# Kernel tuning notes

Measured on AMD Instinct MI355X. Metric: run time of the kernel, lower is better.

The kernel has to match this reference:

```python
import jax, jax.numpy as jnp
import numpy as np

N = 1_000_000          # number of RoIs
C = 4                  # num_class (foreground classes)
IMG_H, IMG_W = 1080.0, 1920.0
BBOX_MEAN = jnp.array([0.0, 0.0, 0.0, 0.0], jnp.float32)
BBOX_STD = jnp.array([0.1, 0.1, 0.2, 0.2], jnp.float32)
THR_OBJ = 0.2          # threshold_objectness
THR_CLS = 0.1          # thresholds[0]
MIN_W, MIN_H = 6.0, 6.0
MAX_CAND = 300         # nms max_candidate_n
OVERLAP = 0.5          # nms overlap_ratio
TOP_N = 100            # nms top_n


def setup_inputs() -> dict:
    key = jax.random.key(0)
    k1, k2, k3, k4, k5 = jax.random.split(key, 5)
    logits = jax.random.normal(k1, (N, C + 1), jnp.float32) * 2.0
    cls_score_softmax = jax.nn.softmax(logits, axis=-1)          # rows sum to 1, like softmax output
    bbox_pred = jax.random.normal(k2, (N, 4 * (C + 1)), jnp.float32) * 0.5
    x1 = jax.random.uniform(k3, (N,), jnp.float32, 0.0, IMG_W * 0.8)
    y1 = jax.random.uniform(k4, (N,), jnp.float32, 0.0, IMG_H * 0.8)
    wh = jax.random.uniform(k5, (N, 2), jnp.float32, 8.0, 200.0)
    rois = jnp.stack([jnp.zeros((N,), jnp.float32), x1, y1, x1 + wh[:, 0], y1 + wh[:, 1]], axis=1)
    im_info = jnp.array([IMG_H, IMG_W], jnp.float32)
    return {"cls_score_softmax": cls_score_softmax, "bbox_pred": bbox_pred, "rois": rois, "im_info": im_info}


def _pairwise_iou(b):
    # torchvision box_iou convention: area = (x2-x1)*(y2-y1), no +1
    lt = jnp.maximum(b[:, None, :2], b[None, :, :2])
    rb = jnp.minimum(b[:, None, 2:], b[None, :, 2:])
    wh = jnp.clip(rb - lt, 0.0)
    inter = wh[..., 0] * wh[..., 1]
    area = (b[:, 2] - b[:, 0]) * (b[:, 3] - b[:, 1])
    return inter / (area[:, None] + area[None, :] - inter)


def _forward(cls_score_softmax, bbox_pred, rois, im_info):
    h_img, w_img = im_info[0], im_info[1]
    # denormalize deltas and decode against rois (bbox_transform_inv_rcnn)
    deltas = (bbox_pred.reshape(-1, 4) * BBOX_STD + BBOX_MEAN).reshape(-1, C + 1, 4)
    bx = rois[:, 1:]
    w = bx[:, 2] - bx[:, 0] + 1.0
    h = bx[:, 3] - bx[:, 1] + 1.0
    cx = bx[:, 0] + 0.5 * (w - 1.0)
    cy = bx[:, 1] + 0.5 * (h - 1.0)
    pcx = deltas[:, :, 0] * w[:, None] + cx[:, None]
    pcy = deltas[:, :, 1] * h[:, None] + cy[:, None]
    pw = jnp.exp(deltas[:, :, 2]) * w[:, None]
    ph = jnp.exp(deltas[:, :, 3]) * h[:, None]
    pred = jnp.stack([pcx - 0.5 * (pw - 1.0), pcy - 0.5 * (ph - 1.0),
                      pcx + 0.5 * (pw - 1.0), pcy + 0.5 * (ph - 1.0)], axis=-1)  # [N, C+1, 4]
    # refine_out_of_map_bbox: clip to image
    pred = jnp.stack([jnp.clip(pred[..., 0], 0.0, w_img - 1.0),
                      jnp.clip(pred[..., 1], 0.0, h_img - 1.0),
                      jnp.clip(pred[..., 2], 0.0, w_img - 1.0),
                      jnp.clip(pred[..., 3], 0.0, h_img - 1.0)], axis=-1)
    # objectness + class-score filters (masked instead of compacted: jit-friendly)
    mask_obj = (1.0 - cls_score_softmax[:, 0]) >= THR_OBJ
    maxes = jnp.max(cls_score_softmax[:, 1:], axis=1)
    argmaxes = jnp.argmax(cls_score_softmax[:, 1:], axis=1) + 1
    mask_cls = maxes > THR_CLS
    # select the box of the argmax class per row
    box = jnp.take_along_axis(pred, argmaxes[:, None, None], axis=1)[:, 0, :]  # [N, 4]
    bw = box[:, 2] - box[:, 0] + 1.0
    bh = box[:, 3] - box[:, 1] + 1.0
    mask_size = (bw >= MIN_W) | (bh >= MIN_H)  # HEIGHT_OR_WIDTH
    valid = mask_obj & mask_cls & mask_size
    # top-k candidates by max class prob (invalid rows pushed below any real score)
    cand_scores = jnp.where(valid, maxes, -1.0)
    top_vals, top_idx = jax.lax.top_k(cand_scores, MAX_CAND)   # sorted descending
    cand_boxes = box[top_idx]                                   # [M, 4]
    cand_probs = cls_score_softmax[top_idx]                     # [M, C+1]
    cand_valid = top_vals > -0.5
    # greedy NMS over the (score-sorted) candidates
    iou = _pairwise_iou(cand_boxes)
    idx = jnp.arange(MAX_CAND)

    def body(i, keep):
        sup = keep[i] & (iou[i] > OVERLAP) & (idx > i)
        return keep & ~sup

    keep = jax.lax.fori_loop(0, MAX_CAND, body, cand_valid)
    # compact kept rows into the first TOP_N slots (drop-row scatter trick)
    order = jnp.cumsum(keep.astype(jnp.int32)) - 1
    slot = jnp.where(keep & (order < TOP_N), order, TOP_N)
    rows = jnp.concatenate([jnp.zeros((MAX_CAND, 1), cand_boxes.dtype), cand_boxes, cand_probs], axis=1)
    out = jnp.zeros((TOP_N + 1, rows.shape[1]), rows.dtype).at[slot].set(rows)[:TOP_N]
    return out  # [TOP_N, 1 + 4 + (C+1)] = [100, 10], zero-padded past the kept count


def reference(cls_score_softmax, bbox_pred, rois, im_info):
    return _forward(cls_score_softmax, bbox_pred, rois, im_info)
```

## Files before the change

### kernel.cpp

```cpp
#include <hip/hip_runtime.h>
#include <math.h>

#define NBINS 4096
#define CAP   4096
#define MAXC  300
#define MAXCP 320
#define NTASK (MAXC*5)
#define TOPN  100

__device__ __forceinline__ void decode4(float x1, float y1, float x2, float y2,
                                        float4 d4, float Wimg, float Himg,
                                        float& bx1, float& by1, float& bx2, float& by2)
{
    float w  = x2 - x1 + 1.0f;
    float h  = y2 - y1 + 1.0f;
    float cx = x1 + 0.5f*(w - 1.0f);
    float cy = y1 + 0.5f*(h - 1.0f);
    float d0 = d4.x*0.1f, d1 = d4.y*0.1f, d2 = d4.z*0.2f, d3 = d4.w*0.2f;
    float pcx = d0*w + cx;
    float pcy = d1*h + cy;
    float pw  = expf(d2)*w;
    float ph  = expf(d3)*h;
    bx1 = fminf(fmaxf(pcx - 0.5f*(pw-1.0f), 0.0f), Wimg-1.0f);
    by1 = fminf(fmaxf(pcy - 0.5f*(ph-1.0f), 0.0f), Himg-1.0f);
    bx2 = fminf(fmaxf(pcx + 0.5f*(pw-1.0f), 0.0f), Wimg-1.0f);
    by2 = fminf(fmaxf(pcy + 0.5f*(ph-1.0f), 0.0f), Himg-1.0f);
}

__global__ __launch_bounds__(256)
void rcnn_pass1(const float4* __restrict__ cls4, const float4* __restrict__ bbox4,
                const float4* __restrict__ rois4, const float* __restrict__ iminfo,
                float4* __restrict__ scores4,
                unsigned int* __restrict__ hist, unsigned int* __restrict__ counter, int Ng)
{
    if (blockIdx.x == 0) {
        for (int k = threadIdx.x; k < NBINS; k += 256) hist[k] = 0u;
        if (threadIdx.x == 0) *counter = 0u;
    }

    int g = blockIdx.x * blockDim.x + threadIdx.x;
    if (g >= Ng) return;

    float c[20], q[20];
    #pragma unroll
    for (int v = 0; v < 5; v++) {
        float4 cv = cls4[5*g + v];
        c[4*v] = cv.x; c[4*v+1] = cv.y; c[4*v+2] = cv.z; c[4*v+3] = cv.w;
        float4 rv = rois4[5*g + v];
        q[4*v] = rv.x; q[4*v+1] = rv.y; q[4*v+2] = rv.z; q[4*v+3] = rv.w;
    }
    float Himg = iminfo[0], Wimg = iminfo[1];

    float s[4];
    #pragma unroll
    for (int j = 0; j < 4; j++) {
        float p0 = c[5*j], p1 = c[5*j+1], p2 = c[5*j+2], p3 = c[5*j+3], p4 = c[5*j+4];
        float m = p1; int a = 1;
        if (p2 > m) { m = p2; a = 2; }
        if (p3 > m) { m = p3; a = 3; }
        if (p4 > m) { m = p4; a = 4; }
        float sc = -1.0f;
        if (((1.0f - p0) >= 0.2f) && (m > 0.1f)) {
            float4 d4 = bbox4[20*g + 5*j + a];
            float bx1, by1, bx2, by2;
            decode4(q[5*j+1], q[5*j+2], q[5*j+3], q[5*j+4], d4, Wimg, Himg, bx1, by1, bx2, by2);
            float bw = bx2 - bx1 + 1.0f;
            float bh = by2 - by1 + 1.0f;
            if ((bw >= 6.0f) || (bh >= 6.0f)) sc = m;
        }
        s[j] = sc;
    }
    scores4[g] = make_float4(s[0], s[1], s[2], s[3]);
}

__global__ __launch_bounds__(1024)
void rcnn_hist(const float4* __restrict__ scores4, unsigned int* __restrict__ hist, int Ng)
{
    __shared__ unsigned int lh[NBINS];
    const int t = threadIdx.x;
    for (int k = t; k < NBINS; k += 1024) lh[k] = 0u;
    __syncthreads();

    int stride = gridDim.x * 1024;
    for (int g = blockIdx.x * 1024 + t; g < Ng; g += stride) {
        float4 s4 = scores4[g];
        float ss[4] = { s4.x, s4.y, s4.z, s4.w };
        #pragma unroll
        for (int j = 0; j < 4; j++) {
            float s = ss[j];
            if (s > -0.5f) {
                int bin = (int)(s * (float)NBINS);
                bin = bin > NBINS-1 ? NBINS-1 : bin;
                atomicAdd(&lh[bin], 1u);
            }
        }
    }
    __syncthreads();
    for (int k = t; k < NBINS; k += 1024) {
        unsigned int v = lh[k];
        if (v) atomicAdd(&hist[k], v);
    }
}

__global__ __launch_bounds__(64)
void rcnn_pass2(const unsigned int* __restrict__ hist, int* __restrict__ taubin)
{
    const int t = threadIdx.x;
    const uint4* h4 = (const uint4*)hist;
    uint4 v[16];
    #pragma unroll
    for (int j = 0; j < 16; j++) v[j] = h4[t*16 + j];
    unsigned int chunk = 0;
    #pragma unroll
    for (int j = 0; j < 16; j++) chunk += v[j].x + v[j].y + v[j].z + v[j].w;

    unsigned int sfx = chunk;
    #pragma unroll
    for (int d = 1; d < 64; d <<= 1) {
        unsigned int o = __shfl_down(sfx, d, 64);
        if (t + d < 64) sfx += o;
    }
    unsigned int nxt = sfx - chunk;
    bool found = (sfx >= MAXC) && (nxt < MAXC);
    unsigned long long bal = __ballot(found);
    if (found) {
        unsigned int cum = nxt;
        int tau = 64*t;
        #pragma unroll
        for (int k = 15; k >= 0; k--) {
            cum += v[k].w; if (cum >= MAXC) { tau = 64*t + 4*k + 3; goto done; }
            cum += v[k].z; if (cum >= MAXC) { tau = 64*t + 4*k + 2; goto done; }
            cum += v[k].y; if (cum >= MAXC) { tau = 64*t + 4*k + 1; goto done; }
            cum += v[k].x; if (cum >= MAXC) { tau = 64*t + 4*k + 0; goto done; }
        }
        done:
        *taubin = tau;
    }
    if (bal == 0ull && t == 0) *taubin = 0;
}

__global__ __launch_bounds__(256)
void rcnn_pass3(const float4* __restrict__ scores4, const int* __restrict__ taubin,
                float* __restrict__ cscore, int* __restrict__ cidx,
                unsigned int* __restrict__ counter, int Ng)
{
    int g = blockIdx.x * blockDim.x + threadIdx.x;
    if (g >= Ng) return;
    float4 s4 = scores4[g];
    int tau = *taubin;
    float ss[4] = { s4.x, s4.y, s4.z, s4.w };
    #pragma unroll
    for (int j = 0; j < 4; j++) {
        float s = ss[j];
        if (s > -0.5f) {
            int bin = (int)(s * (float)NBINS);
            bin = bin > NBINS-1 ? NBINS-1 : bin;
            if (bin >= tau) {
                unsigned int pos = atomicAdd(counter, 1u);
                if (pos < CAP) { cscore[pos] = s; cidx[pos] = 4*g + j; }
            }
        }
    }
}

__global__ __launch_bounds__(1024)
void rcnn_rank(const float* __restrict__ cls, const float* __restrict__ bbox,
               const float* __restrict__ rois, const float* __restrict__ iminfo,
               const float* __restrict__ cscore, const int* __restrict__ cidx,
               const unsigned int* __restrict__ counter,
               float4* __restrict__ bxg, float* __restrict__ areag,
               float* __restrict__ prg, unsigned long long* __restrict__ maskg)
{
    __shared__ __align__(16) float s_s[CAP];
    __shared__ __align__(16) int   s_id[CAP];
    __shared__ int tid_[MAXC];
    __shared__ unsigned long long maskw[5];
    const int t  = threadIdx.x;
    const int NT = 1024;
    int M = (int)*counter; if (M > CAP) M = CAP;

    for (int i = t; i < M; i += NT)  { s_s[i] = cscore[i]; s_id[i] = cidx[i]; }
    for (int r = t; r < MAXC; r += NT) tid_[r] = -1;
    if (t < 5) maskw[t] = 0ull;
    __syncthreads();

    {
        const float4* sv = (const float4*)s_s;
        const int4*   dv = (const int4*)s_id;
        int M4 = M >> 2;
        for (int i = t; i < M; i += NT) {
            float si = s_s[i]; int di = s_id[i];
            int r = 0;
            for (int jj = 0; jj < M4; jj++) {
                float4 sj = sv[jj]; int4 dj = dv[jj];
                r += (sj.x > si) || (sj.x == si && dj.x < di);
                r += (sj.y > si) || (sj.y == si && dj.y < di);
                r += (sj.z > si) || (sj.z == si && dj.z < di);
                r += (sj.w > si) || (sj.w == si && dj.w < di);
            }
            for (int j = M4 << 2; j < M; j++) {
                float sj = s_s[j]; int dj = s_id[j];
                r += (sj > si) || (sj == si && dj < di);
            }
            if (r < MAXC) tid_[r] = di;
        }
    }
    __syncthreads();

    float Himg = iminfo[0], Wimg = iminfo[1];
    for (int r = t; r < MAXCP; r += NT) {
        int i = (r < MAXC) ? tid_[r] : -1;
        float4 bx = make_float4(0.0f, 0.0f, 0.0f, 0.0f);
        float ar = 0.0f;
        if (i >= 0) {
            float p0 = cls[5*i], p1 = cls[5*i+1], p2 = cls[5*i+2], p3 = cls[5*i+3], p4 = cls[5*i+4];
            prg[5*r+0]=p0; prg[5*r+1]=p1; prg[5*r+2]=p2; prg[5*r+3]=p3; prg[5*r+4]=p4;
            float m = p1; int a = 1;
            if (p2 > m) { m = p2; a = 2; }
            if (p3 > m) { m = p3; a = 3; }
            if (p4 > m) { m = p4; a = 4; }
            float4 d4 = ((const float4*)bbox)[5*i + a];
            float bx1, by1, bx2, by2;
            decode4(rois[5*i+1], rois[5*i+2], rois[5*i+3], rois[5*i+4], d4, Wimg, Himg, bx1, by1, bx2, by2);
            bx = make_float4(bx1, by1, bx2, by2);
            ar = (bx2-bx1)*(by2-by1);
            atomicOr(&maskw[r>>6], 1ull << (r & 63));
        }
        bxg[r] = bx; areag[r] = ar;
    }
    __syncthreads();
    if (t < 5) maskg[t] = maskw[t];
}

__global__ __launch_bounds__(64)
void rcnn_sup(const float4* __restrict__ bxg, const float* __restrict__ areag,
              const unsigned long long* __restrict__ maskg,
              unsigned long long* __restrict__ supg)
{
    __shared__ float4 bxs[MAXCP];
    __shared__ float  ars[MAXCP];
    const int t = threadIdx.x;
    for (int r = t; r < MAXCP; r += 64) { bxs[r] = bxg[r]; ars[r] = areag[r]; }
    __syncthreads();

    int task = blockIdx.x * 64 + t;
    if (task >= NTASK) return;
    int w = task / MAXC;
    int i = task - w * MAXC;
    unsigned long long bits = 0ull;
    int j0 = w << 6;
    if (j0 + 63 > i) {
        float4 bi = bxs[i];
        float areaA = ars[i];
        for (int b = 0; b < 64; b++) {
            int j = j0 + b;
            float4 bj = bxs[j];
            float lx = fmaxf(bi.x, bj.x), ly = fmaxf(bi.y, bj.y);
            float rx = fminf(bi.z, bj.z), ry = fminf(bi.w, bj.w);
            float iw = fmaxf(rx - lx, 0.0f), ih = fmaxf(ry - ly, 0.0f);
            float inter = iw * ih;
            float iou = inter / (areaA + ars[j] - inter);
            bits |= (iou > 0.5f) ? (1ull << b) : 0ull;
        }
        unsigned long long jgt = (i < j0) ? ~0ull
                              : ((i - j0) >= 63 ? 0ull : ~((1ull << (i - j0 + 1)) - 1ull));
        bits &= jgt & maskg[w];
    }
    supg[i*6 + w] = bits;
}

__global__ __launch_bounds__(1024)
void rcnn_scan(const float4* __restrict__ bxg, const float* __restrict__ prg,
               const unsigned long long* __restrict__ maskg,
               const unsigned long long* __restrict__ supg, float* __restrict__ out)
{
    __shared__ __align__(16) unsigned long long sup[MAXC*6];
    __shared__ unsigned long long maskw[5];
    __shared__ float orows[TOPN*10];
    __shared__ int   kept_list[TOPN];
    __shared__ int   s_kept;
    const int t  = threadIdx.x;
    const int NT = 1024;

    {
        const ulonglong2* sg2 = (const ulonglong2*)supg;
        ulonglong2* sl2 = (ulonglong2*)sup;
        for (int k = t; k < (MAXC*6)/2; k += NT) sl2[k] = sg2[k];
    }
    if (t < 5) maskw[t] = maskg[t];
    for (int k = t; k < TOPN*10; k += NT) orows[k] = 0.0f;
    __syncthreads();

    if (t == 0) {
        unsigned long long k0=maskw[0], k1=maskw[1], k2=maskw[2], k3=maskw[3], k4=maskw[4];
        int kept = 0;
        #define SCAN_WORD(W, KW)                                                   \
        if (kept < TOPN) {                                                         \
            unsigned long long donem = 0ull;                                       \
            for (;;) {                                                             \
                unsigned long long rem = (KW) & ~donem;                            \
                if (!rem) break;                                                   \
                int b = __builtin_ctzll(rem);                                      \
                int i = (W << 6) + b;                                              \
                kept_list[kept++] = i;                                             \
                if (kept >= TOPN) break;                                           \
                unsigned long long s0 = sup[i*6+0], s1 = sup[i*6+1],               \
                                   s2 = sup[i*6+2], s3 = sup[i*6+3],               \
                                   s4 = sup[i*6+4];                                \
                k0 &= ~s0; k1 &= ~s1; k2 &= ~s2; k3 &= ~s3; k4 &= ~s4;             \
                donem = (b == 63) ? ~0ull : ((2ull << b) - 1ull);                  \
            }                                                                      \
        }
        SCAN_WORD(0, k0)
        SCAN_WORD(1, k1)
        SCAN_WORD(2, k2)
        SCAN_WORD(3, k3)
        SCAN_WORD(4, k4)
        #undef SCAN_WORD
        s_kept = kept;
    }
    __syncthreads();

    int kept = s_kept;
    if (t < kept) {
        int r = kept_list[t];
        float4 bx = bxg[r];
        float* row = &orows[t*10];
        row[0] = 0.0f;
        row[1] = bx.x; row[2] = bx.y; row[3] = bx.z; row[4] = bx.w;
        row[5] = prg[5*r+0]; row[6] = prg[5*r+1]; row[7] = prg[5*r+2];
        row[8] = prg[5*r+3]; row[9] = prg[5*r+4];
    }
    __syncthreads();
    for (int k = t; k < TOPN*10; k += NT) out[k] = orows[k];
}

extern "C" void kernel_launch(void* const* d_in, const int* in_sizes, int n_in,
                              void* d_out, int out_size, void* d_ws, size_t ws_size,
                              hipStream_t stream)
{
    const float* cls    = (const float*)d_in[0];
    const float* bbox   = (const float*)d_in[1];
    const float* rois   = (const float*)d_in[2];
    const float* iminfo = (const float*)d_in[3];
    int N  = in_sizes[0] / 5;
    int Ng = N / 4;

    char* ws = (char*)d_ws;
    float* scores = (float*)ws;
    size_t off = ((size_t)N * 4 + 255) & ~(size_t)255;
    unsigned int* hist    = (unsigned int*)(ws + off); off += NBINS * 4;
    int*          taubin  = (int*)(ws + off);          off += 256;
    unsigned int* counter = (unsigned int*)(ws + off); off += 256;
    float*        cscore  = (float*)(ws + off);        off += CAP * 4;
    int*          cidx    = (int*)(ws + off);          off += CAP * 4;
    float4*       bxg     = (float4*)(ws + off);       off += MAXCP * 16;
    float*        areag   = (float*)(ws + off);        off += ((MAXCP * 4 + 255) & ~(size_t)255);
    float*        prg     = (float*)(ws + off);        off += ((MAXC * 5 * 4 + 255) & ~(size_t)255);
    unsigned long long* maskg = (unsigned long long*)(ws + off); off += 256;
    unsigned long long* supg  = (unsigned long long*)(ws + off); off += MAXC * 6 * 8;

    int blocksG = (Ng + 255) / 256;
    rcnn_pass1<<<blocksG, 256, 0, stream>>>((const float4*)cls, (const float4*)bbox,
                                            (const float4*)rois, iminfo,
                                            (float4*)scores, hist, counter, Ng);
    rcnn_hist<<<64, 1024, 0, stream>>>((const float4*)scores, hist, Ng);
    rcnn_pass2<<<1, 64, 0, stream>>>(hist, taubin);
    rcnn_pass3<<<blocksG, 256, 0, stream>>>((const float4*)scores, taubin,
                                            cscore, cidx, counter, Ng);
    rcnn_rank<<<1, 1024, 0, stream>>>(cls, bbox, rois, iminfo,
                                      cscore, cidx, counter,
                                      bxg, areag, prg, maskg);
    rcnn_sup<<<(NTASK + 63) / 64, 64, 0, stream>>>(bxg, areag, maskg, supg);
    rcnn_scan<<<1, 1024, 0, stream>>>(bxg, prg, maskg, supg, (float*)d_out);
}
```

Before: 206.5 us.

## Fuse seven launches into three using grid-wide atomic tickets and spin barriers

```diff
diff --git a/kernel.cpp b/kernel.cpp
--- a/kernel.cpp
+++ b/kernel.cpp
@@ -7,6 +7,8 @@
 #define MAXCP 320
 #define NTASK (MAXC*5)
 #define TOPN  100
+#define HBLK  64
+#define RBLK  25
 
 __device__ __forceinline__ void decode4(float x1, float y1, float x2, float y2,
                                         float4 d4, float Wimg, float Himg,
@@ -30,17 +32,24 @@
 __global__ __launch_bounds__(256)
 void rcnn_pass1(const float4* __restrict__ cls4, const float4* __restrict__ bbox4,
                 const float4* __restrict__ rois4, const float* __restrict__ iminfo,
-                float4* __restrict__ scores4,
-                unsigned int* __restrict__ hist, unsigned int* __restrict__ counter, int Ng)
+                float4* __restrict__ scores4, unsigned int* __restrict__ hist,
+                int* __restrict__ taubin, unsigned int* __restrict__ hticket,
+                unsigned int* __restrict__ counter, unsigned int* __restrict__ rtick,
+                unsigned int* __restrict__ stick,
+                float4* __restrict__ bxg, float* __restrict__ areag,
+                unsigned long long* __restrict__ maskg, int Ng)
 {
     if (blockIdx.x == 0) {
         for (int k = threadIdx.x; k < NBINS; k += 256) hist[k] = 0u;
-        if (threadIdx.x == 0) *counter = 0u;
-    }
-
+        if (threadIdx.x == 0) { *counter = 0u; *hticket = 0u; *rtick = 0u; *stick = 0u; *taubin = -1; }
+        if (threadIdx.x < 5) maskg[threadIdx.x] = 0ull;
+        for (int r = threadIdx.x; r < MAXCP; r += 256) {
+            bxg[r] = make_float4(0.0f, 0.0f, 0.0f, 0.0f);
+            areag[r] = 0.0f;
+        }
+    }
     int g = blockIdx.x * blockDim.x + threadIdx.x;
     if (g >= Ng) return;
-
     float c[20], q[20];
     #pragma unroll
     for (int v = 0; v < 5; v++) {
@@ -50,7 +59,6 @@
         q[4*v] = rv.x; q[4*v+1] = rv.y; q[4*v+2] = rv.z; q[4*v+3] = rv.w;
     }
     float Himg = iminfo[0], Wimg = iminfo[1];
-
     float s[4];
     #pragma unroll
     for (int j = 0; j < 4; j++) {
@@ -74,13 +82,17 @@
 }
 
 __global__ __launch_bounds__(1024)
-void rcnn_hist(const float4* __restrict__ scores4, unsigned int* __restrict__ hist, int Ng)
+void rcnn_histc(const float4* __restrict__ scores4, unsigned int* __restrict__ hist,
+                unsigned int* __restrict__ hticket, int* __restrict__ taubin,
+                float* __restrict__ cscore, int* __restrict__ cidx,
+                unsigned int* __restrict__ counter, int Ng)
 {
     __shared__ unsigned int lh[NBINS];
+    __shared__ unsigned int s_tick;
+    __shared__ int s_tau;
     const int t = threadIdx.x;
     for (int k = t; k < NBINS; k += 1024) lh[k] = 0u;
     __syncthreads();
-
     int stride = gridDim.x * 1024;
     for (int g = blockIdx.x * 1024 + t; g < Ng; g += stride) {
         float4 s4 = scores4[g];
@@ -100,239 +112,243 @@
         unsigned int v = lh[k];
         if (v) atomicAdd(&hist[k], v);
     }
-}
-
-__global__ __launch_bounds__(64)
-void rcnn_pass2(const unsigned int* __restrict__ hist, int* __restrict__ taubin)
-{
-    const int t = threadIdx.x;
-    const uint4* h4 = (const uint4*)hist;
-    uint4 v[16];
-    #pragma unroll
-    for (int j = 0; j < 16; j++) v[j] = h4[t*16 + j];
-    unsigned int chunk = 0;
-    #pragma unroll
-    for (int j = 0; j < 16; j++) chunk += v[j].x + v[j].y + v[j].z + v[j].w;
-
-    unsigned int sfx = chunk;
-    #pragma unroll
-    for (int d = 1; d < 64; d <<= 1) {
-        unsigned int o = __shfl_down(sfx, d, 64);
-        if (t + d < 64) sfx += o;
-    }
-    unsigned int nxt = sfx - chunk;
-    bool found = (sfx >= MAXC) && (nxt < MAXC);
-    unsigned long long bal = __ballot(found);
-    if (found) {
-        unsigned int cum = nxt;
-        int tau = 64*t;
+
+    __threadfence();
+    __syncthreads();
+    if (t == 0) s_tick = atomicAdd(hticket, 1u);
+    __syncthreads();
+
+    if (s_tick == gridDim.x - 1) {
+        __threadfence();
+        if (t < 64) {
+            const uint4* h4 = (const uint4*)hist;
+            uint4 v[16];
+            #pragma unroll
+            for (int j = 0; j < 16; j++) v[j] = h4[t*16 + j];
+            unsigned int chunk = 0;
+            #pragma unroll
+            for (int j = 0; j < 16; j++) chunk += v[j].x + v[j].y + v[j].z + v[j].w;
+            unsigned int sfx = chunk;
+            #pragma unroll
+            for (int d = 1; d < 64; d <<= 1) {
+                unsigned int o = __shfl_down(sfx, d, 64);
+                if (t + d < 64) sfx += o;
+            }
+            unsigned int nxt = sfx - chunk;
+            bool found = (sfx >= MAXC) && (nxt < MAXC);
+            unsigned long long bal = __ballot(found);
+            if (found) {
+                unsigned int cum = nxt;
+                int tauv = 64*t;
+                #pragma unroll
+                for (int k = 15; k >= 0; k--) {
+                    cum += v[k].w; if (cum >= MAXC) { tauv = 64*t + 4*k + 3; goto dtau; }
+                    cum += v[k].z; if (cum >= MAXC) { tauv = 64*t + 4*k + 2; goto dtau; }
+                    cum += v[k].y; if (cum >= MAXC) { tauv = 64*t + 4*k + 1; goto dtau; }
+                    cum += v[k].x; if (cum >= MAXC) { tauv = 64*t + 4*k + 0; goto dtau; }
+                }
+                dtau:
+                atomicExch(taubin, tauv);
+            }
+            if (bal == 0ull && t == 0) atomicExch(taubin, 0);
+        }
+    }
+
+    if (t == 0) {
+        int tv = atomicAdd(taubin, 0);
+        while (tv < 0) { __builtin_amdgcn_s_sleep(2); tv = atomicAdd(taubin, 0); }
+        s_tau = tv;
+    }
+    __syncthreads();
+    int tau = s_tau;
+
+    for (int g = blockIdx.x * 1024 + t; g < Ng; g += stride) {
+        float4 s4 = scores4[g];
+        float ss[4] = { s4.x, s4.y, s4.z, s4.w };
         #pragma unroll
-        for (int k = 15; k >= 0; k--) {
-            cum += v[k].w; if (cum >= MAXC) { tau = 64*t + 4*k + 3; goto done; }
-            cum += v[k].z; if (cum >= MAXC) { tau = 64*t + 4*k + 2; goto done; }
-            cum += v[k].y; if (cum >= MAXC) { tau = 64*t + 4*k + 1; goto done; }
-            cum += v[k].x; if (cum >= MAXC) { tau = 64*t + 4*k + 0; goto done; }
-        }
-        done:
-        *taubin = tau;
-    }
-    if (bal == 0ull && t == 0) *taubin = 0;
-}
-
-__global__ __launch_bounds__(256)
-void rcnn_pass3(const float4* __restrict__ scores4, const int* __restrict__ taubin,
-                float* __restrict__ cscore, int* __restrict__ cidx,
-                unsigned int* __restrict__ counter, int Ng)
-{
-    int g = blockIdx.x * blockDim.x + threadIdx.x;
-    if (g >= Ng) return;
-    float4 s4 = scores4[g];
-    int tau = *taubin;
-    float ss[4] = { s4.x, s4.y, s4.z, s4.w };
-    #pragma unroll
-    for (int j = 0; j < 4; j++) {
-        float s = ss[j];
-        if (s > -0.5f) {
-            int bin = (int)(s * (float)NBINS);
-            bin = bin > NBINS-1 ? NBINS-1 : bin;
-            if (bin >= tau) {
-                unsigned int pos = atomicAdd(counter, 1u);
-                if (pos < CAP) { cscore[pos] = s; cidx[pos] = 4*g + j; }
+        for (int j = 0; j < 4; j++) {
+            float s = ss[j];
+            if (s > -0.5f) {
+                int bin = (int)(s * (float)NBINS);
+                bin = bin > NBINS-1 ? NBINS-1 : bin;
+                if (bin >= tau) {
+                    unsigned int pos = atomicAdd(counter, 1u);
+                    if (pos < CAP) { cscore[pos] = s; cidx[pos] = 4*g + j; }
+                }
             }
         }
     }
 }
 
 __global__ __launch_bounds__(1024)
-void rcnn_rank(const float* __restrict__ cls, const float* __restrict__ bbox,
-               const float* __restrict__ rois, const float* __restrict__ iminfo,
-               const float* __restrict__ cscore, const int* __restrict__ cidx,
-               const unsigned int* __restrict__ counter,
-               float4* __restrict__ bxg, float* __restrict__ areag,
-               float* __restrict__ prg, unsigned long long* __restrict__ maskg)
-{
-    __shared__ __align__(16) float s_s[CAP];
-    __shared__ __align__(16) int   s_id[CAP];
-    __shared__ int tid_[MAXC];
-    __shared__ unsigned long long maskw[5];
-    const int t  = threadIdx.x;
-    const int NT = 1024;
-    int M = (int)*counter; if (M > CAP) M = CAP;
-
-    for (int i = t; i < M; i += NT)  { s_s[i] = cscore[i]; s_id[i] = cidx[i]; }
-    for (int r = t; r < MAXC; r += NT) tid_[r] = -1;
-    if (t < 5) maskw[t] = 0ull;
-    __syncthreads();
+void rcnn_mega2(const float* __restrict__ cls, const float* __restrict__ bbox,
+                const float* __restrict__ rois, const float* __restrict__ iminfo,
+                const float* __restrict__ cscore, const int* __restrict__ cidx,
+                const unsigned int* __restrict__ counter,
+                unsigned int* __restrict__ rtick, unsigned int* __restrict__ stick,
+                float4* __restrict__ bxg, float* __restrict__ areag,
+                float* __restrict__ prg, unsigned long long* __restrict__ maskg,
+                unsigned long long* __restrict__ supg, float* __restrict__ out)
+{
+    __shared__ __align__(16) unsigned char u[32768];
+    __shared__ float orows[TOPN*10];
+    __shared__ int   kept_list[TOPN];
+    __shared__ int   s_kept;
+    const int t   = threadIdx.x;
+    const int bid = blockIdx.x;
 
     {
+        float* s_s  = (float*)u;
+        int*   s_id = (int*)(u + CAP*4);
+        int M = (int)*counter; if (M > CAP) M = CAP;
+        for (int i = t; i < M; i += 1024) { s_s[i] = cscore[i]; s_id[i] = cidx[i]; }
+        __syncthreads();
+        int C = (M + RBLK - 1) / RBLK;
+        float Himg = iminfo[0], Wimg = iminfo[1];
         const float4* sv = (const float4*)s_s;
         const int4*   dv = (const int4*)s_id;
         int M4 = M >> 2;
-        for (int i = t; i < M; i += NT) {
-            float si = s_s[i]; int di = s_id[i];
-            int r = 0;
-            for (int jj = 0; jj < M4; jj++) {
-                float4 sj = sv[jj]; int4 dj = dv[jj];
-                r += (sj.x > si) || (sj.x == si && dj.x < di);
-                r += (sj.y > si) || (sj.y == si && dj.y < di);
-                r += (sj.z > si) || (sj.z == si && dj.z < di);
-                r += (sj.w > si) || (sj.w == si && dj.w < di);
-            }
-            for (int j = M4 << 2; j < M; j++) {
-                float sj = s_s[j]; int dj = s_id[j];
-                r += (sj > si) || (sj == si && dj < di);
-            }
-            if (r < MAXC) tid_[r] = di;
-        }
-    }
-    __syncthreads();
-
-    float Himg = iminfo[0], Wimg = iminfo[1];
-    for (int r = t; r < MAXCP; r += NT) {
-        int i = (r < MAXC) ? tid_[r] : -1;
-        float4 bx = make_float4(0.0f, 0.0f, 0.0f, 0.0f);
-        float ar = 0.0f;
-        if (i >= 0) {
-            float p0 = cls[5*i], p1 = cls[5*i+1], p2 = cls[5*i+2], p3 = cls[5*i+3], p4 = cls[5*i+4];
-            prg[5*r+0]=p0; prg[5*r+1]=p1; prg[5*r+2]=p2; prg[5*r+3]=p3; prg[5*r+4]=p4;
-            float m = p1; int a = 1;
-            if (p2 > m) { m = p2; a = 2; }
-            if (p3 > m) { m = p3; a = 3; }
-            if (p4 > m) { m = p4; a = 4; }
-            float4 d4 = ((const float4*)bbox)[5*i + a];
-            float bx1, by1, bx2, by2;
-            decode4(rois[5*i+1], rois[5*i+2], rois[5*i+3], rois[5*i+4], d4, Wimg, Himg, bx1, by1, bx2, by2);
-            bx = make_float4(bx1, by1, bx2, by2);
-            ar = (bx2-bx1)*(by2-by1);
-            atomicOr(&maskw[r>>6], 1ull << (r & 63));
-        }
-        bxg[r] = bx; areag[r] = ar;
-    }
-    __syncthreads();
-    if (t < 5) maskg[t] = maskw[t];
-}
-
-__global__ __launch_bounds__(64)
-void rcnn_sup(const float4* __restrict__ bxg, const float* __restrict__ areag,
-              const unsigned long long* __restrict__ maskg,
-              unsigned long long* __restrict__ supg)
-{
-    __shared__ float4 bxs[MAXCP];
-    __shared__ float  ars[MAXCP];
-    const int t = threadIdx.x;
-    for (int r = t; r < MAXCP; r += 64) { bxs[r] = bxg[r]; ars[r] = areag[r]; }
-    __syncthreads();
-
-    int task = blockIdx.x * 64 + t;
-    if (task >= NTASK) return;
-    int w = task / MAXC;
-    int i = task - w * MAXC;
-    unsigned long long bits = 0ull;
-    int j0 = w << 6;
-    if (j0 + 63 > i) {
-        float4 bi = bxs[i];
-        float areaA = ars[i];
-        for (int b = 0; b < 64; b++) {
-            int j = j0 + b;
-            float4 bj = bxs[j];
-            float lx = fmaxf(bi.x, bj.x), ly = fmaxf(bi.y, bj.y);
-            float rx = fminf(bi.z, bj.z), ry = fminf(bi.w, bj.w);
-            float iw = fmaxf(rx - lx, 0.0f), ih = fmaxf(ry - ly, 0.0f);
-            float inter = iw * ih;
-            float iou = inter / (areaA + ars[j] - inter);
-            bits |= (iou > 0.5f) ? (1ull << b) : 0ull;
-        }
-        unsigned long long jgt = (i < j0) ? ~0ull
-                              : ((i - j0) >= 63 ? 0ull : ~((1ull << (i - j0 + 1)) - 1ull));
-        bits &= jgt & maskg[w];
-    }
-    supg[i*6 + w] = bits;
-}
-
-__global__ __launch_bounds__(1024)
-void rcnn_scan(const float4* __restrict__ bxg, const float* __restrict__ prg,
-               const unsigned long long* __restrict__ maskg,
-               const unsigned long long* __restrict__ supg, float* __restrict__ out)
-{
-    __shared__ __align__(16) unsigned long long sup[MAXC*6];
-    __shared__ unsigned long long maskw[5];
-    __shared__ float orows[TOPN*10];
-    __shared__ int   kept_list[TOPN];
-    __shared__ int   s_kept;
-    const int t  = threadIdx.x;
-    const int NT = 1024;
+        for (int ii = t; ii < C; ii += 1024) {
+            int i = bid * C + ii;
+            if (i < M) {
+                float si = s_s[i]; int di = s_id[i];
+                int r = 0;
+                for (int jj = 0; jj < M4; jj++) {
+                    float4 sj = sv[jj]; int4 dj = dv[jj];
+                    r += (sj.x > si) || (sj.x == si && dj.x < di);
+                    r += (sj.y > si) || (sj.y == si && dj.y < di);
+                    r += (sj.z > si) || (sj.z == si && dj.z < di);
+                    r += (sj.w > si) || (sj.w == si && dj.w < di);
+                }
+                for (int j = M4 << 2; j < M; j++) {
+                    float sj = s_s[j]; int dj = s_id[j];
+                    r += (sj > si) || (sj == si && dj < di);
+                }
+                if (r < MAXC) {
+                    int idx = di;
+                    float p0 = cls[5*idx], p1 = cls[5*idx+1], p2 = cls[5*idx+2],
+                          p3 = cls[5*idx+3], p4 = cls[5*idx+4];
+                    prg[5*r+0]=p0; prg[5*r+1]=p1; prg[5*r+2]=p2; prg[5*r+3]=p3; prg[5*r+4]=p4;
+                    float m = p1; int a = 1;
+                    if (p2 > m) { m = p2; a = 2; }
+                    if (p3 > m) { m = p3; a = 3; }
+                    if (p4 > m) { m = p4; a = 4; }
+                    float4 d4 = ((const float4*)bbox)[5*idx + a];
+                    float bx1, by1, bx2, by2;
+                    decode4(rois[5*idx+1], rois[5*idx+2], rois[5*idx+3], rois[5*idx+4],
+                            d4, Wimg, Himg, bx1, by1, bx2, by2);
+                    bxg[r] = make_float4(bx1, by1, bx2, by2);
+                    areag[r] = (bx2-bx1)*(by2-by1);
+                    atomicOr(&maskg[r>>6], 1ull << (r & 63));
+                }
+            }
+        }
+    }
+    __threadfence();
+    __syncthreads();
+    if (t == 0) {
+        atomicAdd(rtick, 1u);
+        unsigned int v = atomicAdd(rtick, 0u);
+        while (v < RBLK) { __builtin_amdgcn_s_sleep(2); v = atomicAdd(rtick, 0u); }
+    }
+    __syncthreads();
+    __threadfence();
 
     {
+        float4* bxs = (float4*)u;
+        float*  ars = (float*)(u + MAXCP*16);
+        for (int r = t; r < MAXCP; r += 1024) { bxs[r] = bxg[r]; ars[r] = areag[r]; }
+        __syncthreads();
+        if (bid < 24 && t < 64) {
+            int task = bid * 64 + t;
+            if (task < NTASK) {
+                int w = task / MAXC;
+                int i = task - w * MAXC;
+                unsigned long long bits = 0ull;
+                int j0 = w << 6;
+                if (j0 + 63 > i) {
+                    float4 bi = bxs[i];
+                    float areaA = ars[i];
+                    for (int b = 0; b < 64; b++) {
+                        int j = j0 + b;
+                        float4 bj = bxs[j];
+                        float lx = fmaxf(bi.x, bj.x), ly = fmaxf(bi.y, bj.y);
+                        float rx = fminf(bi.z, bj.z), ry = fminf(bi.w, bj.w);
+                        float iw = fmaxf(rx - lx, 0.0f), ih = fmaxf(ry - ly, 0.0f);
+                        float inter = iw * ih;
+                        float iou = inter / (areaA + ars[j] - inter);
+                        bits |= (iou > 0.5f) ? (1ull << b) : 0ull;
+                    }
+                    unsigned long long jgt = (i < j0) ? ~0ull
+                                          : ((i - j0) >= 63 ? 0ull : ~((1ull << (i - j0 + 1)) - 1ull));
+                    bits &= jgt & maskg[w];
+                }
+                supg[i*6 + w] = bits;
+            }
+        }
+    }
+    __threadfence();
+    __syncthreads();
+    if (t == 0) atomicAdd(stick, 1u);
+    if (bid != 0) return;
+    if (t == 0) {
+        unsigned int v = atomicAdd(stick, 0u);
+        while (v < RBLK) { __builtin_amdgcn_s_sleep(2); v = atomicAdd(stick, 0u); }
+    }
+    __syncthreads();
+    __threadfence();
+
+    {
+        unsigned long long* sup = (unsigned long long*)u;
         const ulonglong2* sg2 = (const ulonglong2*)supg;
         ulonglong2* sl2 = (ulonglong2*)sup;
-        for (int k = t; k < (MAXC*6)/2; k += NT) sl2[k] = sg2[k];
-    }
-    if (t < 5) maskw[t] = maskg[t];
-    for (int k = t; k < TOPN*10; k += NT) orows[k] = 0.0f;
-    __syncthreads();
-
-    if (t == 0) {
-        unsigned long long k0=maskw[0], k1=maskw[1], k2=maskw[2], k3=maskw[3], k4=maskw[4];
-        int kept = 0;
-        #define SCAN_WORD(W, KW)                                                   \
-        if (kept < TOPN) {                                                         \
-            unsigned long long donem = 0ull;                                       \
-            for (;;) {                                                             \
-                unsigned long long rem = (KW) & ~donem;                            \
-                if (!rem) break;                                                   \
-                int b = __builtin_ctzll(rem);                                      \
-                int i = (W << 6) + b;                                              \
-                kept_list[kept++] = i;                                             \
-                if (kept >= TOPN) break;                                           \
-                unsigned long long s0 = sup[i*6+0], s1 = sup[i*6+1],               \
-                                   s2 = sup[i*6+2], s3 = sup[i*6+3],               \
-                                   s4 = sup[i*6+4];                                \
-                k0 &= ~s0; k1 &= ~s1; k2 &= ~s2; k3 &= ~s3; k4 &= ~s4;             \
-                donem = (b == 63) ? ~0ull : ((2ull << b) - 1ull);                  \
-            }                                                                      \
-        }
-        SCAN_WORD(0, k0)
-        SCAN_WORD(1, k1)
-        SCAN_WORD(2, k2)
-        SCAN_WORD(3, k3)
-        SCAN_WORD(4, k4)
-        #undef SCAN_WORD
-        s_kept = kept;
-    }
-    __syncthreads();
-
-    int kept = s_kept;
-    if (t < kept) {
-        int r = kept_list[t];
-        float4 bx = bxg[r];
-        float* row = &orows[t*10];
-        row[0] = 0.0f;
-        row[1] = bx.x; row[2] = bx.y; row[3] = bx.z; row[4] = bx.w;
-        row[5] = prg[5*r+0]; row[6] = prg[5*r+1]; row[7] = prg[5*r+2];
-        row[8] = prg[5*r+3]; row[9] = prg[5*r+4];
-    }
-    __syncthreads();
-    for (int k = t; k < TOPN*10; k += NT) out[k] = orows[k];
+        for (int k = t; k < (MAXC*6)/2; k += 1024) sl2[k] = sg2[k];
+        for (int k = t; k < TOPN*10; k += 1024) orows[k] = 0.0f;
+        __syncthreads();
+
+        if (t == 0) {
+            unsigned long long k0=maskg[0], k1=maskg[1], k2=maskg[2], k3=maskg[3], k4=maskg[4];
+            int kept = 0;
+            #define SCAN_WORD(W, KW)                                                   \
+            if (kept < TOPN) {                                                         \
+                unsigned long long donem = 0ull;                                       \
+                for (;;) {                                                             \
+                    unsigned long long rem = (KW) & ~donem;                            \
+                    if (!rem) break;                                                   \
+                    int b = __builtin_ctzll(rem);                                      \
+                    int i = (W << 6) + b;                                              \
+                    kept_list[kept++] = i;                                             \
+                    if (kept >= TOPN) break;                                           \
+                    unsigned long long s0 = sup[i*6+0], s1 = sup[i*6+1],               \
+                                       s2 = sup[i*6+2], s3 = sup[i*6+3],               \
+                                       s4 = sup[i*6+4];                                \
+                    k0 &= ~s0; k1 &= ~s1; k2 &= ~s2; k3 &= ~s3; k4 &= ~s4;             \
+                    donem = (b == 63) ? ~0ull : ((2ull << b) - 1ull);                  \
+                }                                                                      \
+            }
+            SCAN_WORD(0, k0)
+            SCAN_WORD(1, k1)
+            SCAN_WORD(2, k2)
+            SCAN_WORD(3, k3)
+            SCAN_WORD(4, k4)
+            #undef SCAN_WORD
+            s_kept = kept;
+        }
+        __syncthreads();
+
+        int kept = s_kept;
+        if (t < kept) {
+            int r = kept_list[t];
+            float4 bx = bxg[r];
+            float* row = &orows[t*10];
+            row[0] = 0.0f;
+            row[1] = bx.x; row[2] = bx.y; row[3] = bx.z; row[4] = bx.w;
+            row[5] = prg[5*r+0]; row[6] = prg[5*r+1]; row[7] = prg[5*r+2];
+            row[8] = prg[5*r+3]; row[9] = prg[5*r+4];
+        }
+        __syncthreads();
+        for (int k = t; k < TOPN*10; k += 1024) out[k] = orows[k];
+    }
 }
 
 extern "C" void kernel_launch(void* const* d_in, const int* in_sizes, int n_in,
@@ -350,8 +366,11 @@
     float* scores = (float*)ws;
     size_t off = ((size_t)N * 4 + 255) & ~(size_t)255;
     unsigned int* hist    = (unsigned int*)(ws + off); off += NBINS * 4;
-    int*          taubin  = (int*)(ws + off);          off += 256;
-    unsigned int* counter = (unsigned int*)(ws + off); off += 256;
+    int*          taubin  = (int*)(ws + off);          off += 64;
+    unsigned int* hticket = (unsigned int*)(ws + off); off += 64;
+    unsigned int* counter = (unsigned int*)(ws + off); off += 64;
+    unsigned int* rtick   = (unsigned int*)(ws + off); off += 64;
+    unsigned int* stick   = (unsigned int*)(ws + off); off += 256;
     float*        cscore  = (float*)(ws + off);        off += CAP * 4;
     int*          cidx    = (int*)(ws + off);          off += CAP * 4;
     float4*       bxg     = (float4*)(ws + off);       off += MAXCP * 16;
@@ -363,14 +382,11 @@
     int blocksG = (Ng + 255) / 256;
     rcnn_pass1<<<blocksG, 256, 0, stream>>>((const float4*)cls, (const float4*)bbox,
                                             (const float4*)rois, iminfo,
-                                            (float4*)scores, hist, counter, Ng);
-    rcnn_hist<<<64, 1024, 0, stream>>>((const float4*)scores, hist, Ng);
-    rcnn_pass2<<<1, 64, 0, stream>>>(hist, taubin);
-    rcnn_pass3<<<blocksG, 256, 0, stream>>>((const float4*)scores, taubin,
-                                            cscore, cidx, counter, Ng);
-    rcnn_rank<<<1, 1024, 0, stream>>>(cls, bbox, rois, iminfo,
-                                      cscore, cidx, counter,
-                                      bxg, areag, prg, maskg);
-    rcnn_sup<<<(NTASK + 63) / 64, 64, 0, stream>>>(bxg, areag, maskg, supg);
-    rcnn_scan<<<1, 1024, 0, stream>>>(bxg, prg, maskg, supg, (float*)d_out);
-}
+                                            (float4*)scores, hist, taubin, hticket,
+                                            counter, rtick, stick, bxg, areag, maskg, Ng);
+    rcnn_histc<<<HBLK, 1024, 0, stream>>>((const float4*)scores, hist, hticket, taubin,
+                                          cscore, cidx, counter, Ng);
+    rcnn_mega2<<<RBLK, 1024, 0, stream>>>(cls, bbox, rois, iminfo, cscore, cidx, counter,
+                                          rtick, stick, bxg, areag, prg, maskg, supg,
+                                          (float*)d_out);
+}
```

After: 236.4 us. +14.5%, slower.
